# Optimization experiments

Hardware: AMD Instinct MI355X
Metric: run time of the kernel (lower is better)

Reference implementation:

```python
import jax, jax.numpy as jnp
import numpy as np

N, T, D, H, NH, BS = 4, 4096, 512, 8, 4, 64
DH = D // H                 # head dim = 64
NB = T // BS                # n_buckets = 64
CS = NH * NB                # chunk_size = 256
L = NH * T                  # sorted sequence length per head


def setup_inputs() -> dict:
    key = jax.random.key(0)
    ks = jax.random.split(key, 4)
    x = jax.random.normal(ks[0], (N, T, D), jnp.float32)
    W_Q = jax.random.normal(ks[1], (D, D), jnp.float32) * (D ** -0.5)
    W_V = jax.random.normal(ks[2], (D, D), jnp.float32) * (D ** -0.5)
    b_Q = jnp.zeros((D,), jnp.float32)
    b_V = jnp.zeros((D,), jnp.float32)
    gamma = jnp.ones((D,), jnp.float32)
    beta = jnp.zeros((D,), jnp.float32)
    # per-head random rotations: (dim_head, num_hashes, n_buckets // 2)
    rotations = jax.random.normal(ks[3], (H, DH, NH, NB // 2), jnp.float32)
    return {"x": x, "W_Q": W_Q, "b_Q": b_Q, "W_V": W_V, "b_V": b_V,
            "gamma": gamma, "beta": beta, "rotations": rotations}


def _look_one_back(a):
    # concat each chunk with the previous chunk (wrap-around for chunk 0)
    extra = jnp.concatenate([a[:, -1:], a[:, :-1]], axis=1)
    return jnp.concatenate([a, extra], axis=2)


def _lsh_head(qk, v, rot):
    # qk, v: [N, T, DH]; rot: [DH, NH, NB//2]
    rotated = jnp.einsum('btf,fhi->bhti', qk, rot)               # [N,NH,T,NB//2]
    rotated = jnp.concatenate([rotated, -rotated], axis=-1)       # [N,NH,T,NB]
    buckets = jnp.argmax(rotated, axis=-1)                        # [N,NH,T]
    offsets = (jnp.arange(NH) * NB)[None, :, None]
    buckets = (buckets + offsets).reshape(N, L)                   # [N, NH*T]

    ticker = jnp.broadcast_to(jnp.arange(L)[None, :], (N, L))
    buckets_and_t = T * buckets + (ticker % T)                    # unique keys
    sticker = jnp.argsort(buckets_and_t, axis=-1)                 # sorted ticker ids
    undo_sort = jnp.argsort(sticker, axis=-1)
    st = sticker % T                                              # original positions

    sqk = jnp.take_along_axis(qk, st[..., None], axis=1)          # [N,L,DH]
    sv = jnp.take_along_axis(v, st[..., None], axis=1)

    bq_t = st.reshape(N, CS, -1)                                  # [N,CS,BS]
    bqk = sqk.reshape(N, CS, -1, DH)
    bv = sv.reshape(N, CS, -1, DH)
    bq = bqk
    bk = bqk / (jnp.linalg.norm(bqk, axis=-1, keepdims=True) + 1e-6)

    bk = _look_one_back(bk)                                       # [N,CS,2*BS,DH]
    bv = _look_one_back(bv)
    bkv_t = _look_one_back(bq_t)

    dots = jnp.einsum('bcie,bcje->bcij', bq, bk) * (DH ** -0.5)   # [N,CS,BS,2BS]

    # mask out pairs hashed to different buckets
    q_sb = jnp.take_along_axis(buckets, sticker, axis=1).reshape(N, CS, -1)
    kv_sb = _look_one_back(q_sb)
    dots = jnp.where(q_sb[:, :, :, None] != kv_sb[:, :, None, :], -1e9, dots)
    # down-weight self-attention (same position)
    dots = jnp.where(bq_t[:, :, :, None] == bkv_t[:, :, None, :], -1e-5, dots)

    lse = jax.nn.logsumexp(dots, axis=-1, keepdims=True)
    probs = jnp.exp(dots - lse)
    bo = jnp.einsum('bcij,bcje->bcie', probs, bv)                 # [N,CS,BS,DH]

    so = bo.reshape(N, L, DH)
    slog = lse.reshape(N, L)
    o = jnp.take_along_axis(so, undo_sort[..., None], axis=1)
    logits = jnp.take_along_axis(slog, undo_sort, axis=1)

    o = o.reshape(N, NH, T, DH)
    logits = logits.reshape(N, NH, T, 1)
    pw = jnp.exp(logits - jax.nn.logsumexp(logits, axis=1, keepdims=True))
    return jnp.sum(o * pw, axis=1)                                # [N,T,DH]


def reference(x, W_Q, b_Q, W_V, b_V, gamma, beta, rotations):
    Q = x @ W_Q + b_Q
    V = x @ W_V + b_V
    Qh = Q.reshape(N, T, H, DH).transpose(2, 0, 1, 3)             # [H,N,T,DH]
    Vh = V.reshape(N, T, H, DH).transpose(2, 0, 1, 3)
    outs = jax.vmap(_lsh_head)(Qh, Vh, rotations)                 # [H,N,T,DH]
    out = outs.transpose(1, 2, 0, 3).reshape(N, T, D)
    mu = out.mean(axis=-1, keepdims=True)
    var = out.var(axis=-1, keepdims=True)
    return gamma * (out - mu) / jnp.sqrt(var + 1e-3) + beta
```

## Files before the change

### kernel.cpp

```cpp
#include <hip/hip_runtime.h>
#include <hip/hip_bf16.h>

#define N_ 4
#define T_ 4096
#define D_ 512
#define H_ 8
#define DH_ 64
#define NH_ 4
#define NB_ 64
#define CS_ 256
#define L_ 16384

typedef unsigned short u16;
typedef unsigned int u32;
typedef __attribute__((ext_vector_type(8))) short short8;
typedef __attribute__((ext_vector_type(8))) _Float16 half8;
typedef __attribute__((ext_vector_type(4))) float f32x4;
typedef __attribute__((ext_vector_type(2))) float f32x2;

__device__ __forceinline__ u16 f2bf(float x){
    union { float f; u32 u; } c; c.f = x;
    u32 u = c.u;
    u32 r = (u + 0x7FFFu + ((u >> 16) & 1u)) >> 16;
    return (u16)r;
}
__device__ __forceinline__ float bf2f(u16 b){
    union { u32 u; float f; } c; c.u = ((u32)b) << 16;
    return c.f;
}
__device__ __forceinline__ u16 f2h(float x){
    _Float16 h = (_Float16)x;
    u16 r; __builtin_memcpy(&r, &h, 2); return r;
}

#define PK_LO(acc, a, b) \
    asm("v_pk_fma_f32 %0, %1, %2, %0 op_sel:[0,0,0] op_sel_hi:[0,1,1]" \
        : "+v"(acc) : "v"(a), "v"(b))
#define PK_HI(acc, a, b) \
    asm("v_pk_fma_f32 %0, %1, %2, %0 op_sel:[1,0,0] op_sel_hi:[1,1,1]" \
        : "+v"(acc) : "v"(a), "v"(b))

#define VSWZ(d) ((((d) >> 3) ^ ((d) & 7)))

__global__ __launch_bounds__(256) void k_decXf(const float* __restrict__ x,
        u16* __restrict__ xf){
    int i = blockIdx.x * 256 + threadIdx.x;
    float4 v = ((const float4*)x)[i];
    ushort4 o;
    o.x = f2h(v.x); o.y = f2h(v.y); o.z = f2h(v.z); o.w = f2h(v.w);
    ((ushort4*)xf)[i] = o;
}

__global__ __launch_bounds__(256) void k_decWv(const float* __restrict__ Wv,
        u16* __restrict__ wvt){
    __shared__ float tile[32][33];
    const int tid = threadIdx.x;
    const int kt = blockIdx.x * 32, nt = blockIdx.y * 32;
    const int tx = tid & 31, ty = tid >> 5;
    #pragma unroll
    for (int i = 0; i < 4; ++i)
        tile[ty + i * 8][tx] = Wv[(size_t)(kt + ty + i * 8) * 512 + nt + tx];
    __syncthreads();
    #pragma unroll
    for (int i = 0; i < 4; ++i){
        int n = ty + i * 8;
        wvt[(size_t)(nt + n) * 512 + kt + tx] = f2h(tile[tx][n]);
    }
}

__global__ __launch_bounds__(512, 4) void k_q(const float* __restrict__ x,
        const float* __restrict__ Wq, const float* __restrict__ bq,
        float* __restrict__ Q, u16* __restrict__ Qbf, float* __restrict__ qinv){
    __shared__ float sA[2][16][132];
    __shared__ float sB[2][16][132];
    const int tid = threadIdx.x;
    const int tx = tid & 31, ty = tid >> 5;
    const int mb = blockIdx.x * 128, nb = blockIdx.y * 128;

    f32x2 acc2[8][2];
    #pragma unroll
    for (int i = 0; i < 8; ++i){
        acc2[i][0] = (f32x2){0.f, 0.f};
        acc2[i][1] = (f32x2){0.f, 0.f};
    }

    const int mA = tid >> 2, kA = (tid & 3) * 4;
    const int kB = tid >> 5, cB = (tid & 31) * 4;
    const float* xp = &x[(size_t)(mb + mA) * 512 + kA];
    const float* wp = &Wq[(size_t)kB * 512 + nb + cB];

    float4 pa = *(const float4*)xp;
    float4 pb = *(const float4*)wp;

    for (int k0 = 0; k0 < 512; k0 += 16){
        const int p = (k0 >> 4) & 1;
        sA[p][kA + 0][mA] = pa.x; sA[p][kA + 1][mA] = pa.y;
        sA[p][kA + 2][mA] = pa.z; sA[p][kA + 3][mA] = pa.w;
        *(float4*)&sB[p][kB][cB] = pb;
        __syncthreads();
        if (k0 < 496){
            pa = *(const float4*)(xp + k0 + 16);
            pb = *(const float4*)(wp + (size_t)(k0 + 16) * 512);
        }
        #pragma unroll
        for (int kk = 0; kk < 16; ++kk){
            float4 va0 = *(const float4*)&sA[p][kk][ty * 8];
            float4 va1 = *(const float4*)&sA[p][kk][ty * 8 + 4];
            float4 vb  = *(const float4*)&sB[p][kk][tx * 4];
            f32x2 a2[4], b2[2];
            a2[0] = (f32x2){va0.x, va0.y}; a2[1] = (f32x2){va0.z, va0.w};
            a2[2] = (f32x2){va1.x, va1.y}; a2[3] = (f32x2){va1.z, va1.w};
            b2[0] = (f32x2){vb.x, vb.y};   b2[1] = (f32x2){vb.z, vb.w};
            #pragma unroll
            for (int i = 0; i < 8; ++i){
                if (i & 1){
                    PK_HI(acc2[i][0], a2[i >> 1], b2[0]);
                    PK_HI(acc2[i][1], a2[i >> 1], b2[1]);
                } else {
                    PK_LO(acc2[i][0], a2[i >> 1], b2[0]);
                    PK_LO(acc2[i][1], a2[i >> 1], b2[1]);
                }
            }
        }
    }

    float4 vbq = *(const float4*)&bq[nb + tx * 4];
    const int h = blockIdx.y * 2 + (tx >> 4);
    const int d0 = (tx & 15) * 4;
    #pragma unroll
    for (int i = 0; i < 8; ++i){
        float o0 = acc2[i][0].x + vbq.x;
        float o1 = acc2[i][0].y + vbq.y;
        float o2 = acc2[i][1].x + vbq.z;
        float o3 = acc2[i][1].y + vbq.w;
        int m = mb + ty * 8 + i;
        int n = m >> 12, t = m & (T_ - 1);
        float4 q4; q4.x = o0; q4.y = o1; q4.z = o2; q4.w = o3;
        *(float4*)&Q[(size_t)m * 512 + nb + tx * 4] = q4;
        float ss = o0 * o0 + o1 * o1 + o2 * o2 + o3 * o3;
        #pragma unroll
        for (int s = 8; s >= 1; s >>= 1) ss += __shfl_xor(ss, s, 64);
        size_t rowb = (size_t)(h * N_ + n) * T_ + t;
        if ((tx & 15) == 0) qinv[rowb] = 1.f / (sqrtf(ss) + 1e-6f);
        ushort4 qb4;
        qb4.x = f2bf(o0); qb4.y = f2bf(o1); qb4.z = f2bf(o2); qb4.w = f2bf(o3);
        *(ushort4*)&Qbf[rowb * 64 + d0] = qb4;
    }
}

__global__ __launch_bounds__(256) void k_gemmV(const u16* __restrict__ xf,
        const u16* __restrict__ wvt, const float* __restrict__ bv,
        u16* __restrict__ Vbf){
    __shared__ __align__(16) u16 sA[128 * 40];
    __shared__ __align__(16) u16 sB[128 * 40];
    const int tid = threadIdx.x;
    const int mb = blockIdx.x * 128, nb = blockIdx.y * 128;
    const int w = tid >> 6, lane = tid & 63, quad = lane >> 4, cc = lane & 15;
    const int wm = (w & 1) * 64, wn = (w >> 1) * 64;
    f32x4 acc[4][4];
    #pragma unroll
    for (int i = 0; i < 4; ++i)
        #pragma unroll
        for (int j = 0; j < 4; ++j) acc[i][j] = (f32x4){0.f, 0.f, 0.f, 0.f};

    for (int k0 = 0; k0 < 512; k0 += 32){
        #pragma unroll
        for (int i = 0; i < 2; ++i){
            int idx = i * 256 + tid;
            int m = idx >> 2, ks = idx & 3;
            *(short8*)&sA[m * 40 + ks * 8] =
                *(const short8*)&xf[(size_t)(mb + m) * 512 + k0 + ks * 8];
            *(short8*)&sB[m * 40 + ks * 8] =
                *(const short8*)&wvt[(size_t)(nb + m) * 512 + k0 + ks * 8];
        }
        __syncthreads();
        half8 a[4], b[4];
        #pragma unroll
        for (int i = 0; i < 4; ++i){
            a[i] = *(const half8*)&sA[(wm + i * 16 + cc) * 40 + quad * 8];
            b[i] = *(const half8*)&sB[(wn + i * 16 + cc) * 40 + quad * 8];
        }
        #pragma unroll
        for (int i = 0; i < 4; ++i)
            #pragma unroll
            for (int j = 0; j < 4; ++j)
                acc[i][j] = __builtin_amdgcn_mfma_f32_16x16x32_f16(a[i], b[j], acc[i][j], 0, 0, 0);
        __syncthreads();
    }
    #pragma unroll
    for (int i = 0; i < 4; ++i)
        #pragma unroll
        for (int j = 0; j < 4; ++j){
            int c = nb + wn + j * 16 + cc;
            int hh = c >> 6, d = c & 63;
            float bi = bv[c];
            #pragma unroll
            for (int r = 0; r < 4; ++r){
                int m = mb + wm + i * 16 + quad * 4 + r;
                int n = m >> 12, t = m & (T_ - 1);
                Vbf[((size_t)(hh * N_ + n) * T_ + t) * 64 + d] = f2bf(acc[i][j][r] + bi);
            }
        }
}

__global__ __launch_bounds__(256) void k_rot(const float* __restrict__ Q,
        const float* __restrict__ rot, int* __restrict__ buckets){
    const int tb = blockIdx.x * 32;
    const int n = blockIdx.y, h = blockIdx.z;
    const int hn = h * N_ + n;
    __shared__ float Rs[64 * 128];
    __shared__ float Qs[32][64];
    const int tid = threadIdx.x;
    const float* rh = rot + (size_t)h * (64 * 128);
    for (int idx = tid; idx < 8192; idx += 256){
        int f = idx >> 7, rem = idx & 127, jj = rem >> 5, i2 = rem & 31;
        Rs[f * 128 + i2 * 4 + jj] = rh[idx];
    }
    for (int i = tid; i < 2048; i += 256){
        int t = i >> 6, f = i & 63;
        Qs[t][f] = Q[(size_t)(n * T_ + tb + t) * 512 + h * 64 + f];
    }
    __syncthreads();
    const int tx = tid & 31, tg = tid >> 5;
    f32x2 r2[4][2];
    #pragma unroll
    for (int tt = 0; tt < 4; ++tt){
        r2[tt][0] = (f32x2){0.f, 0.f};
        r2[tt][1] = (f32x2){0.f, 0.f};
    }
    for (int f = 0; f < 64; f += 2){
        f32x2 qf[4];
        #pragma unroll
        for (int tt = 0; tt < 4; ++tt)
            qf[tt] = *(const f32x2*)&Qs[tg * 4 + tt][f];
        float4 rv0 = *(const float4*)&Rs[f * 128 + tx * 4];
        float4 rv1 = *(const float4*)&Rs[(f + 1) * 128 + tx * 4];
        f32x2 b0[2], b1[2];
        b0[0] = (f32x2){rv0.x, rv0.y}; b0[1] = (f32x2){rv0.z, rv0.w};
        b1[0] = (f32x2){rv1.x, rv1.y}; b1[1] = (f32x2){rv1.z, rv1.w};
        #pragma unroll
        for (int tt = 0; tt < 4; ++tt){
            PK_LO(r2[tt][0], qf[tt], b0[0]);
            PK_LO(r2[tt][1], qf[tt], b0[1]);
            PK_HI(r2[tt][0], qf[tt], b1[0]);
            PK_HI(r2[tt][1], qf[tt], b1[1]);
        }
    }
    #pragma unroll
    for (int tt = 0; tt < 4; ++tt){
        #pragma unroll
        for (int jj = 0; jj < 4; ++jj){
            float rval = (jj < 2) ? r2[tt][0][jj] : r2[tt][1][jj - 2];
            float bv = rval; int bi = tx;
            float nv = -bv;
            if (nv > bv){ bv = nv; bi = 32 + tx; }
            #pragma unroll
            for (int m = 16; m >= 1; m >>= 1){
                float ov = __shfl_xor(bv, m, 32);
                int   oi = __shfl_xor(bi, m, 32);
                if (ov > bv || (ov == bv && oi < bi)){ bv = ov; bi = oi; }
            }
            if (tx == 0){
                int t = tb + tg * 4 + tt;
                buckets[(size_t)hn * L_ + jj * T_ + t] = bi + jj * 64;
            }
        }
    }
}

__global__ __launch_bounds__(256) void k_hist(const int* __restrict__ buckets,
        int* __restrict__ hist){
    const int tile = blockIdx.x, hn = blockIdx.y;
    const int tid = threadIdx.x;
    __shared__ int h[256];
    h[tid] = 0;
    __syncthreads();
    int b = buckets[(size_t)hn * L_ + tile * 256 + tid];
    atomicAdd(&h[b], 1);
    __syncthreads();
    hist[((size_t)hn * 64 + tile) * 256 + tid] = h[tid];
}

__global__ __launch_bounds__(256) void k_scan(int* __restrict__ hist,
        int* __restrict__ bucketStart){
    const int hn = blockIdx.x;
    const int b = threadIdx.x;
    int* hh = hist + (size_t)hn * 64 * 256;
    int run = 0;
    for (int tl = 0; tl < 64; ++tl){
        int v = hh[tl * 256 + b];
        hh[tl * 256 + b] = run;
        run += v;
    }
    __shared__ int s[256];
    s[b] = run;
    __syncthreads();
    for (int off = 1; off < 256; off <<= 1){
        int add = (b >= off) ? s[b - off] : 0;
        __syncthreads();
        s[b] += add;
        __syncthreads();
    }
    bucketStart[hn * 256 + b] = s[b] - run;
}

__global__ __launch_bounds__(256) void k_scatter(const int* __restrict__ buckets,
        const int* __restrict__ offs, const int* __restrict__ bucketStart,
        int* __restrict__ sticker){
    const int tile = blockIdx.x, hn = blockIdx.y;
    const int tid = threadIdx.x;
    __shared__ int sb[256];
    const int i = tile * 256 + tid;
    const int b = buckets[(size_t)hn * L_ + i];
    sb[tid] = b;
    __syncthreads();
    int rank = 0;
    #pragma unroll 8
    for (int j = 0; j < 256; ++j){
        int v = sb[j];
        rank += (j < tid && v == b) ? 1 : 0;
    }
    int pos = bucketStart[hn * 256 + b]
            + offs[((size_t)hn * 64 + tile) * 256 + b]
            + rank;
    sticker[(size_t)hn * L_ + pos] = i;
}

__global__ __launch_bounds__(256) void k_attn(const u16* __restrict__ Qbf,
        const u16* __restrict__ Vbf, const float* __restrict__ qinv,
        const int* __restrict__ buckets, const int* __restrict__ sticker,
        u16* __restrict__ o_hash, float* __restrict__ logit_hash){
    const int blk_c = blockIdx.x, n = blockIdx.y, h = blockIdx.z;
    const int hn = h * N_ + n;
    const int tid = threadIdx.x;
    const int w = tid >> 6, lane = tid & 63;
    const int quad = lane >> 4, cc = lane & 15;

    __shared__ __align__(16) u16 sQP[128 * 64];
    __shared__ __align__(16) u16 sVt[64 * 128];
    __shared__ int s_idx[128], s_buck[128], s_t[128];
    __shared__ float s_inv[128];
    __shared__ float s_lse[64];
    u16* const sQ = sQP;
    u16* const sP = sQP;

    if (tid < 128){
        int cprev = (blk_c + CS_ - 1) & (CS_ - 1);
        int pos = (tid < 64) ? blk_c * 64 + tid : cprev * 64 + (tid - 64);
        int idx = sticker[(size_t)hn * L_ + pos];
        s_idx[tid] = idx;
        s_buck[tid] = buckets[(size_t)hn * L_ + idx];
        int t = idx & (T_ - 1);
        s_t[tid] = t;
        s_inv[tid] = qinv[(size_t)hn * T_ + t] * 0.125f;
    }
    __syncthreads();

    const int r0 = tid >> 3, l8 = tid & 7;
    #pragma unroll
    for (int it = 0; it < 4; ++it){
        int r = it * 32 + r0;
        size_t gb = ((size_t)hn * T_ + s_t[r]) * 64 + l8 * 8;
        short8 qv = *(const short8*)&Qbf[gb];
        *(short8*)&sQ[r * 64 + ((l8 ^ (r & 7)) * 8)] = qv;
        short8 vv = *(const short8*)&Vbf[gb];
        #pragma unroll
        for (int i = 0; i < 8; ++i){
            int d = l8 * 8 + i;
            sVt[d * 128 + (((r >> 3) ^ VSWZ(d)) * 8) + (r & 7)] = (u16)vv[i];
        }
    }
    __syncthreads();

    f32x4 dacc[8];
    #pragma unroll
    for (int j = 0; j < 8; ++j) dacc[j] = (f32x4){0.f, 0.f, 0.f, 0.f};
    const int qrow = w * 16 + cc;
    #pragma unroll
    for (int kc = 0; kc < 2; ++kc){
        short8 afrag = *(const short8*)&sQ[qrow * 64 + (((kc * 4 + quad) ^ (cc & 7)) * 8)];
        #pragma unroll
        for (int kt = 0; kt < 8; ++kt){
            int krow = kt * 16 + cc;
            short8 bfrag = *(const short8*)&sQ[krow * 64 + (((kc * 4 + quad) ^ (cc & 7)) * 8)];
            dacc[kt] = __builtin_amdgcn_mfma_f32_16x16x32_bf16(afrag, bfrag, dacc[kt], 0, 0, 0);
        }
    }

    int bq[4], tq[4];
    #pragma unroll
    for (int r = 0; r < 4; ++r){
        int q = w * 16 + quad * 4 + r;
        bq[r] = s_buck[q]; tq[r] = s_t[q];
    }
    float mrow[4] = {-1e30f, -1e30f, -1e30f, -1e30f};
    #pragma unroll
    for (int kt = 0; kt < 8; ++kt){
        int kk = kt * 16 + cc;
        float inv = s_inv[kk];
        int bk = s_buck[kk], tk = s_t[kk];
        #pragma unroll
        for (int r = 0; r < 4; ++r){
            float d = dacc[kt][r] * inv;
            if (bk != bq[r]) d = -1e9f;
            if (tk == tq[r]) d = -1e-5f;
            dacc[kt][r] = d;
            mrow[r] = fmaxf(mrow[r], d);
        }
    }
    #pragma unroll
    for (int r = 0; r < 4; ++r)
        #pragma unroll
        for (int m = 8; m >= 1; m >>= 1)
            mrow[r] = fmaxf(mrow[r], __shfl_xor(mrow[r], m, 64));
    float srow[4] = {0.f, 0.f, 0.f, 0.f};
    #pragma unroll
    for (int kt = 0; kt < 8; ++kt)
        #pragma unroll
        for (int r = 0; r < 4; ++r){
            float e = __expf(dacc[kt][r] - mrow[r]);
            dacc[kt][r] = e;
            srow[r] += e;
        }
    #pragma unroll
    for (int r = 0; r < 4; ++r)
        #pragma unroll
        for (int m = 8; m >= 1; m >>= 1)
            srow[r] += __shfl_xor(srow[r], m, 64);
    float lse[4], pscale[4];
    #pragma unroll
    for (int r = 0; r < 4; ++r){
        lse[r] = mrow[r] + __logf(srow[r]);
        pscale[r] = 1.f / srow[r];
    }
    if (cc == 0){
        #pragma unroll
        for (int r = 0; r < 4; ++r) s_lse[w * 16 + quad * 4 + r] = lse[r];
    }

    __syncthreads();

    #pragma unroll
    for (int kt = 0; kt < 8; ++kt){
        int kk = kt * 16 + cc;
        #pragma unroll
        for (int r = 0; r < 4; ++r){
            int q = w * 16 + quad * 4 + r;
            sP[q * 128 + (((kk >> 3) ^ (q & 15)) * 8) + (kk & 7)] =
                f2bf(dacc[kt][r] * pscale[r]);
        }
    }
    __syncthreads();

    f32x4 oacc[4];
    #pragma unroll
    for (int j = 0; j < 4; ++j) oacc[j] = (f32x4){0.f, 0.f, 0.f, 0.f};
    #pragma unroll
    for (int kc = 0; kc < 4; ++kc){
        short8 afrag = *(const short8*)&sP[qrow * 128 + (((kc * 4 + quad) ^ cc) * 8)];
        #pragma unroll
        for (int nt = 0; nt < 4; ++nt){
            int d = nt * 16 + cc;
            short8 bfrag = *(const short8*)&sVt[d * 128 + (((kc * 4 + quad) ^ VSWZ(d)) * 8)];
            oacc[nt] = __builtin_amdgcn_mfma_f32_16x16x32_bf16(afrag, bfrag, oacc[nt], 0, 0, 0);
        }
    }

    #pragma unroll
    for (int r = 0; r < 4; ++r){
        int q = w * 16 + quad * 4 + r;
        int si = s_idx[q];
        int jj = si >> 12; int t = si & (T_ - 1);
        size_t base = ((size_t)(hn * NH_ + jj) * T_ + t) * 64;
        #pragma unroll
        for (int nt = 0; nt < 4; ++nt)
            o_hash[base + nt * 16 + cc] = f2bf(oacc[nt][r]);
    }
    if (tid < 64){
        int si = s_idx[tid]; int jj = si >> 12; int t = si & (T_ - 1);
        logit_hash[(size_t)(hn * NH_ + jj) * T_ + t] = s_lse[tid];
    }
}

__global__ __launch_bounds__(256) void k_comb(const u16* __restrict__ o_hash,
        const float* __restrict__ logit_hash, const float* __restrict__ gamma,
        const float* __restrict__ beta, float* __restrict__ out){
    const int t = blockIdx.x, n = blockIdx.y;
    const int tid = threadIdx.x;
    __shared__ float s_pw[32];
    __shared__ float s_x[512];
    __shared__ float s_red[8];
    __shared__ float s_mu, s_rs;
    if (tid < 32){
        int h = tid >> 2, j = tid & 3;
        s_pw[tid] = logit_hash[(size_t)((h * N_ + n) * NH_ + j) * T_ + t];
    }
    __syncthreads();
    if (tid < 8){
        int h = tid;
        float m = -1e30f;
        #pragma unroll
        for (int j = 0; j < 4; ++j) m = fmaxf(m, s_pw[h * 4 + j]);
        float l = 0.f;
        #pragma unroll
        for (int j = 0; j < 4; ++j) l += __expf(s_pw[h * 4 + j] - m);
        float ls = m + __logf(l);
        #pragma unroll
        for (int j = 0; j < 4; ++j) s_pw[h * 4 + j] = __expf(s_pw[h * 4 + j] - ls);
    }
    __syncthreads();
    float va[2];
    #pragma unroll
    for (int i = 0; i < 2; ++i){
        int cidx = tid + i * 256;
        int h = cidx >> 6, d = cidx & 63;
        size_t base = (size_t)((h * N_ + n) * NH_) * T_ * 64;
        float acc = 0.f;
        #pragma unroll
        for (int j = 0; j < 4; ++j)
            acc += s_pw[h * 4 + j] * bf2f(o_hash[base + ((size_t)j * T_ + t) * 64 + d]);
        s_x[cidx] = acc; va[i] = acc;
    }
    float s1 = va[0] + va[1];
    float s2 = va[0] * va[0] + va[1] * va[1];
    #pragma unroll
    for (int m = 32; m >= 1; m >>= 1){
        s1 += __shfl_xor(s1, m, 64);
        s2 += __shfl_xor(s2, m, 64);
    }
    const int lane = tid & 63, w = tid >> 6;
    if (lane == 0){ s_red[w] = s1; s_red[4 + w] = s2; }
    __syncthreads();
    if (tid == 0){
        float S1 = s_red[0] + s_red[1] + s_red[2] + s_red[3];
        float S2 = s_red[4] + s_red[5] + s_red[6] + s_red[7];
        float mu = S1 / 512.f;
        float var = S2 / 512.f - mu * mu;
        s_mu = mu; s_rs = 1.f / sqrtf(var + 1e-3f);
    }
    __syncthreads();
    #pragma unroll
    for (int i = 0; i < 2; ++i){
        int cidx = tid + i * 256;
        out[((size_t)(n * T_ + t)) * 512 + cidx] =
            gamma[cidx] * (s_x[cidx] - s_mu) * s_rs + beta[cidx];
    }
}

extern "C" void kernel_launch(void* const* d_in, const int* in_sizes, int n_in,
                              void* d_out, int out_size, void* d_ws, size_t ws_size,
                              hipStream_t stream){
    const float* x     = (const float*)d_in[0];
    const float* Wq    = (const float*)d_in[1];
    const float* bq    = (const float*)d_in[2];
    const float* Wv    = (const float*)d_in[3];
    const float* bv    = (const float*)d_in[4];
    const float* gamma = (const float*)d_in[5];
    const float* beta  = (const float*)d_in[6];
    const float* rot   = (const float*)d_in[7];
    char* ws = (char*)d_ws;
    float* Q        = (float*)(ws + 0);
    u16*   o_hash   = (u16*)  (ws + 0);
    u16*   Qbf      = (u16*)  (ws + 67108864);
    u16*   Vbf      = (u16*)  (ws + 83886080);
    float* qinv     = (float*)(ws + 100663296);
    int*   buckets  = (int*)  (ws + 101187584);
    int*   sticker  = (int*)  (ws + 103284736);
    float* logit    = (float*)(ws + 105381888);
    int*   hist     = (int*)  (ws + 107479040);
    int*   bstart   = (int*)  (ws + 109576192);
    u16*   xf       = (u16*)  (ws + 109608960);
    u16*   wvt      = (u16*)  (ws + 126386176);

    hipLaunchKernelGGL(k_decXf,   dim3(8192),       dim3(256), 0, stream,
                       x, xf);
    hipLaunchKernelGGL(k_decWv,   dim3(16, 16),     dim3(256), 0, stream,
                       Wv, wvt);
    hipLaunchKernelGGL(k_gemmV,   dim3(128, 4),     dim3(256), 0, stream,
                       xf, wvt, bv, Vbf);
    hipLaunchKernelGGL(k_q,       dim3(128, 4),     dim3(512), 0, stream,
                       x, Wq, bq, Q, Qbf, qinv);
    hipLaunchKernelGGL(k_rot,     dim3(128, 4, 8),  dim3(256), 0, stream,
                       Q, rot, buckets);
    hipLaunchKernelGGL(k_hist,    dim3(64, 32),     dim3(256), 0, stream,
                       buckets, hist);
    hipLaunchKernelGGL(k_scan,    dim3(32),         dim3(256), 0, stream,
                       hist, bstart);
    hipLaunchKernelGGL(k_scatter, dim3(64, 32),     dim3(256), 0, stream,
                       buckets, hist, bstart, sticker);
    hipLaunchKernelGGL(k_attn,    dim3(256, 4, 8),  dim3(256), 0, stream,
                       Qbf, Vbf, qinv, buckets, sticker, o_hash, logit);
    hipLaunchKernelGGL(k_comb,    dim3(4096, 4),    dim3(256), 0, stream,
                       o_hash, logit, gamma, beta, (float*)d_out);
}
```

Measured before the change: 381.0 us.

## Fuse LSH rotation and bucket argmax into the Q projection epilogue

The Q GEMM kernel now keeps its fp32 output tile in shared memory and computes the random-rotation projections and bucket argmax for its two heads directly, removing the separate rotation kernel. This drops the fp32 Q write to global memory and its re-read, plus one kernel launch. In exchange the Q kernel uses more shared memory and adds per-block reloads of the rotation matrices and extra synchronisation, which may reduce occupancy.

```diff
diff --git a/kernel.cpp b/kernel.cpp
--- a/kernel.cpp
+++ b/kernel.cpp
@@ -70,12 +70,20 @@
 
 __global__ __launch_bounds__(512, 4) void k_q(const float* __restrict__ x,
         const float* __restrict__ Wq, const float* __restrict__ bq,
-        float* __restrict__ Q, u16* __restrict__ Qbf, float* __restrict__ qinv){
-    __shared__ float sA[2][16][132];
-    __shared__ float sB[2][16][132];
+        const float* __restrict__ rot, u16* __restrict__ Qbf,
+        float* __restrict__ qinv, int* __restrict__ buckets){
+    __shared__ __align__(16) float uLDS[16640];
+    typedef float (*panel_t)[16][132];
+    panel_t sA = (panel_t)uLDS;
+    panel_t sB = (panel_t)(uLDS + 4224);
+    typedef float (*qs_t)[132];
+    qs_t Qs = (qs_t)uLDS;
+    float* Rs = uLDS + 8448;
+
     const int tid = threadIdx.x;
     const int tx = tid & 31, ty = tid >> 5;
     const int mb = blockIdx.x * 128, nb = blockIdx.y * 128;
+    const int h0 = blockIdx.y * 2;
 
     f32x2 acc2[8][2];
     #pragma unroll
@@ -125,26 +133,102 @@
     }
 
     float4 vbq = *(const float4*)&bq[nb + tx * 4];
-    const int h = blockIdx.y * 2 + (tx >> 4);
-    const int d0 = (tx & 15) * 4;
     #pragma unroll
     for (int i = 0; i < 8; ++i){
-        float o0 = acc2[i][0].x + vbq.x;
-        float o1 = acc2[i][0].y + vbq.y;
-        float o2 = acc2[i][1].x + vbq.z;
-        float o3 = acc2[i][1].y + vbq.w;
-        int m = mb + ty * 8 + i;
-        int n = m >> 12, t = m & (T_ - 1);
-        float4 q4; q4.x = o0; q4.y = o1; q4.z = o2; q4.w = o3;
-        *(float4*)&Q[(size_t)m * 512 + nb + tx * 4] = q4;
-        float ss = o0 * o0 + o1 * o1 + o2 * o2 + o3 * o3;
-        #pragma unroll
-        for (int s = 8; s >= 1; s >>= 1) ss += __shfl_xor(ss, s, 64);
-        size_t rowb = (size_t)(h * N_ + n) * T_ + t;
-        if ((tx & 15) == 0) qinv[rowb] = 1.f / (sqrtf(ss) + 1e-6f);
-        ushort4 qb4;
-        qb4.x = f2bf(o0); qb4.y = f2bf(o1); qb4.z = f2bf(o2); qb4.w = f2bf(o3);
-        *(ushort4*)&Qbf[rowb * 64 + d0] = qb4;
+        acc2[i][0].x += vbq.x; acc2[i][0].y += vbq.y;
+        acc2[i][1].x += vbq.z; acc2[i][1].y += vbq.w;
+    }
+
+    {
+        const int h = h0 + (tx >> 4);
+        const int d0 = (tx & 15) * 4;
+        #pragma unroll
+        for (int i = 0; i < 8; ++i){
+            float o0 = acc2[i][0].x, o1 = acc2[i][0].y;
+            float o2 = acc2[i][1].x, o3 = acc2[i][1].y;
+            int m = mb + ty * 8 + i;
+            int n = m >> 12, t = m & (T_ - 1);
+            float ss = o0 * o0 + o1 * o1 + o2 * o2 + o3 * o3;
+            #pragma unroll
+            for (int s = 8; s >= 1; s >>= 1) ss += __shfl_xor(ss, s, 64);
+            size_t rowb = (size_t)(h * N_ + n) * T_ + t;
+            if ((tx & 15) == 0) qinv[rowb] = 1.f / (sqrtf(ss) + 1e-6f);
+            ushort4 qb4;
+            qb4.x = f2bf(o0); qb4.y = f2bf(o1); qb4.z = f2bf(o2); qb4.w = f2bf(o3);
+            *(ushort4*)&Qbf[rowb * 64 + d0] = qb4;
+        }
+    }
+
+    __syncthreads();
+    const int gi = tid & 31, gg = tid >> 5;
+    #pragma unroll
+    for (int chunk = 0; chunk < 2; ++chunk){
+        if ((ty >> 3) == chunk){
+            const int lt0 = (ty & 7) * 8;
+            #pragma unroll
+            for (int i = 0; i < 8; ++i){
+                float4 q4;
+                q4.x = acc2[i][0].x; q4.y = acc2[i][0].y;
+                q4.z = acc2[i][1].x; q4.w = acc2[i][1].y;
+                *(float4*)&Qs[lt0 + i][tx * 4] = q4;
+            }
+        }
+        #pragma unroll
+        for (int head = 0; head < 2; ++head){
+            const float* rh = rot + (size_t)(h0 + head) * 8192;
+            for (int idx = tid; idx < 8192; idx += 512){
+                int f = idx >> 7, rem = idx & 127, jj = rem >> 5, i2 = rem & 31;
+                Rs[f * 128 + i2 * 4 + jj] = rh[idx];
+            }
+            __syncthreads();
+            f32x2 r2[4][2];
+            #pragma unroll
+            for (int tt = 0; tt < 4; ++tt){
+                r2[tt][0] = (f32x2){0.f, 0.f};
+                r2[tt][1] = (f32x2){0.f, 0.f};
+            }
+            for (int f = 0; f < 64; f += 2){
+                f32x2 qf[4];
+                #pragma unroll
+                for (int tt = 0; tt < 4; ++tt)
+                    qf[tt] = *(const f32x2*)&Qs[gg * 4 + tt][head * 64 + f];
+                float4 rv0 = *(const float4*)&Rs[f * 128 + gi * 4];
+                float4 rv1 = *(const float4*)&Rs[(f + 1) * 128 + gi * 4];
+                f32x2 b0[2], b1[2];
+                b0[0] = (f32x2){rv0.x, rv0.y}; b0[1] = (f32x2){rv0.z, rv0.w};
+                b1[0] = (f32x2){rv1.x, rv1.y}; b1[1] = (f32x2){rv1.z, rv1.w};
+                #pragma unroll
+                for (int tt = 0; tt < 4; ++tt){
+                    PK_LO(r2[tt][0], qf[tt], b0[0]);
+                    PK_LO(r2[tt][1], qf[tt], b0[1]);
+                    PK_HI(r2[tt][0], qf[tt], b1[0]);
+                    PK_HI(r2[tt][1], qf[tt], b1[1]);
+                }
+            }
+            #pragma unroll
+            for (int tt = 0; tt < 4; ++tt){
+                #pragma unroll
+                for (int jj = 0; jj < 4; ++jj){
+                    float rval = (jj < 2) ? r2[tt][0][jj] : r2[tt][1][jj - 2];
+                    float bv = rval; int bi = gi;
+                    float nv = -bv;
+                    if (nv > bv){ bv = nv; bi = 32 + gi; }
+                    #pragma unroll
+                    for (int m = 16; m >= 1; m >>= 1){
+                        float ov = __shfl_xor(bv, m, 32);
+                        int   oi = __shfl_xor(bi, m, 32);
+                        if (ov > bv || (ov == bv && oi < bi)){ bv = ov; bi = oi; }
+                    }
+                    if (gi == 0){
+                        int m = mb + chunk * 64 + gg * 4 + tt;
+                        int nn = m >> 12, t = m & (T_ - 1);
+                        buckets[(size_t)((h0 + head) * N_ + nn) * L_ + jj * T_ + t]
+                            = bi + jj * 64;
+                    }
+                }
+            }
+            __syncthreads();
+        }
     }
 }
 
@@ -201,71 +285,6 @@
                 Vbf[((size_t)(hh * N_ + n) * T_ + t) * 64 + d] = f2bf(acc[i][j][r] + bi);
             }
         }
-}
-
-__global__ __launch_bounds__(256) void k_rot(const float* __restrict__ Q,
-        const float* __restrict__ rot, int* __restrict__ buckets){
-    const int tb = blockIdx.x * 32;
-    const int n = blockIdx.y, h = blockIdx.z;
-    const int hn = h * N_ + n;
-    __shared__ float Rs[64 * 128];
-    __shared__ float Qs[32][64];
-    const int tid = threadIdx.x;
-    const float* rh = rot + (size_t)h * (64 * 128);
-    for (int idx = tid; idx < 8192; idx += 256){
-        int f = idx >> 7, rem = idx & 127, jj = rem >> 5, i2 = rem & 31;
-        Rs[f * 128 + i2 * 4 + jj] = rh[idx];
-    }
-    for (int i = tid; i < 2048; i += 256){
-        int t = i >> 6, f = i & 63;
-        Qs[t][f] = Q[(size_t)(n * T_ + tb + t) * 512 + h * 64 + f];
-    }
-    __syncthreads();
-    const int tx = tid & 31, tg = tid >> 5;
-    f32x2 r2[4][2];
-    #pragma unroll
-    for (int tt = 0; tt < 4; ++tt){
-        r2[tt][0] = (f32x2){0.f, 0.f};
-        r2[tt][1] = (f32x2){0.f, 0.f};
-    }
-    for (int f = 0; f < 64; f += 2){
-        f32x2 qf[4];
-        #pragma unroll
-        for (int tt = 0; tt < 4; ++tt)
-            qf[tt] = *(const f32x2*)&Qs[tg * 4 + tt][f];
-        float4 rv0 = *(const float4*)&Rs[f * 128 + tx * 4];
-        float4 rv1 = *(const float4*)&Rs[(f + 1) * 128 + tx * 4];
-        f32x2 b0[2], b1[2];
-        b0[0] = (f32x2){rv0.x, rv0.y}; b0[1] = (f32x2){rv0.z, rv0.w};
-        b1[0] = (f32x2){rv1.x, rv1.y}; b1[1] = (f32x2){rv1.z, rv1.w};
-        #pragma unroll
-        for (int tt = 0; tt < 4; ++tt){
-            PK_LO(r2[tt][0], qf[tt], b0[0]);
-            PK_LO(r2[tt][1], qf[tt], b0[1]);
-            PK_HI(r2[tt][0], qf[tt], b1[0]);
-            PK_HI(r2[tt][1], qf[tt], b1[1]);
-        }
-    }
-    #pragma unroll
-    for (int tt = 0; tt < 4; ++tt){
-        #pragma unroll
-        for (int jj = 0; jj < 4; ++jj){
-            float rval = (jj < 2) ? r2[tt][0][jj] : r2[tt][1][jj - 2];
-            float bv = rval; int bi = tx;
-            float nv = -bv;
-            if (nv > bv){ bv = nv; bi = 32 + tx; }
-            #pragma unroll
-            for (int m = 16; m >= 1; m >>= 1){
-                float ov = __shfl_xor(bv, m, 32);
-                int   oi = __shfl_xor(bi, m, 32);
-                if (ov > bv || (ov == bv && oi < bi)){ bv = ov; bi = oi; }
-            }
-            if (tx == 0){
-                int t = tb + tg * 4 + tt;
-                buckets[(size_t)hn * L_ + jj * T_ + t] = bi + jj * 64;
-            }
-        }
-    }
 }
 
 __global__ __launch_bounds__(256) void k_hist(const int* __restrict__ buckets,
@@ -559,7 +578,6 @@
     const float* beta  = (const float*)d_in[6];
     const float* rot   = (const float*)d_in[7];
     char* ws = (char*)d_ws;
-    float* Q        = (float*)(ws + 0);
     u16*   o_hash   = (u16*)  (ws + 0);
     u16*   Qbf      = (u16*)  (ws + 67108864);
     u16*   Vbf      = (u16*)  (ws + 83886080);
@@ -579,9 +597,7 @@
     hipLaunchKernelGGL(k_gemmV,   dim3(128, 4),     dim3(256), 0, stream,
                        xf, wvt, bv, Vbf);
     hipLaunchKernelGGL(k_q,       dim3(128, 4),     dim3(512), 0, stream,
-                       x, Wq, bq, Q, Qbf, qinv);
-    hipLaunchKernelGGL(k_rot,     dim3(128, 4, 8),  dim3(256), 0, stream,
-                       Q, rot, buckets);
+                       x, Wq, bq, rot, Qbf, qinv, buckets);
     hipLaunchKernelGGL(k_hist,    dim3(64, 32),     dim3(256), 0, stream,
                        buckets, hist);
     hipLaunchKernelGGL(k_scan,    dim3(32),         dim3(256), 0, stream,
```

Result: slower. 392.1 us (+2.9%).

## Fuse Q and V projection GEMMs into one role-split kernel, convert x inline

Applied to the files above, without the earlier changes.

Removes the separate x-to-fp16 conversion kernel by converting fp32 x to half while staging it into LDS in the V GEMM. Merges the fp32 Q GEMM and the MFMA V GEMM into one launch whose blocks take either role based on block index, so both GEMMs can run concurrently on the device. This drops two launches and an intermediate buffer round trip. In exchange, V blocks waste half their 512 threads, the V path reads fp32 x (twice the bytes), and the shared LDS allocation may limit occupancy.

```diff
diff --git a/kernel.cpp b/kernel.cpp
--- a/kernel.cpp
+++ b/kernel.cpp
@@ -42,15 +42,6 @@
 
 #define VSWZ(d) ((((d) >> 3) ^ ((d) & 7)))
 
-__global__ __launch_bounds__(256) void k_decXf(const float* __restrict__ x,
-        u16* __restrict__ xf){
-    int i = blockIdx.x * 256 + threadIdx.x;
-    float4 v = ((const float4*)x)[i];
-    ushort4 o;
-    o.x = f2h(v.x); o.y = f2h(v.y); o.z = f2h(v.z); o.w = f2h(v.w);
-    ((ushort4*)xf)[i] = o;
-}
-
 __global__ __launch_bounds__(256) void k_decWv(const float* __restrict__ Wv,
         u16* __restrict__ wvt){
     __shared__ float tile[32][33];
@@ -68,139 +59,152 @@
     }
 }
 
-__global__ __launch_bounds__(512, 4) void k_q(const float* __restrict__ x,
+__global__ __launch_bounds__(512, 4) void k_qv(const float* __restrict__ x,
         const float* __restrict__ Wq, const float* __restrict__ bq,
-        float* __restrict__ Q, u16* __restrict__ Qbf, float* __restrict__ qinv){
-    __shared__ float sA[2][16][132];
-    __shared__ float sB[2][16][132];
-    const int tid = threadIdx.x;
-    const int tx = tid & 31, ty = tid >> 5;
-    const int mb = blockIdx.x * 128, nb = blockIdx.y * 128;
-
-    f32x2 acc2[8][2];
-    #pragma unroll
-    for (int i = 0; i < 8; ++i){
-        acc2[i][0] = (f32x2){0.f, 0.f};
-        acc2[i][1] = (f32x2){0.f, 0.f};
-    }
-
-    const int mA = tid >> 2, kA = (tid & 3) * 4;
-    const int kB = tid >> 5, cB = (tid & 31) * 4;
-    const float* xp = &x[(size_t)(mb + mA) * 512 + kA];
-    const float* wp = &Wq[(size_t)kB * 512 + nb + cB];
-
-    float4 pa = *(const float4*)xp;
-    float4 pb = *(const float4*)wp;
-
-    for (int k0 = 0; k0 < 512; k0 += 16){
-        const int p = (k0 >> 4) & 1;
-        sA[p][kA + 0][mA] = pa.x; sA[p][kA + 1][mA] = pa.y;
-        sA[p][kA + 2][mA] = pa.z; sA[p][kA + 3][mA] = pa.w;
-        *(float4*)&sB[p][kB][cB] = pb;
-        __syncthreads();
-        if (k0 < 496){
-            pa = *(const float4*)(xp + k0 + 16);
-            pb = *(const float4*)(wp + (size_t)(k0 + 16) * 512);
-        }
-        #pragma unroll
-        for (int kk = 0; kk < 16; ++kk){
-            float4 va0 = *(const float4*)&sA[p][kk][ty * 8];
-            float4 va1 = *(const float4*)&sA[p][kk][ty * 8 + 4];
-            float4 vb  = *(const float4*)&sB[p][kk][tx * 4];
-            f32x2 a2[4], b2[2];
-            a2[0] = (f32x2){va0.x, va0.y}; a2[1] = (f32x2){va0.z, va0.w};
-            a2[2] = (f32x2){va1.x, va1.y}; a2[3] = (f32x2){va1.z, va1.w};
-            b2[0] = (f32x2){vb.x, vb.y};   b2[1] = (f32x2){vb.z, vb.w};
-            #pragma unroll
-            for (int i = 0; i < 8; ++i){
-                if (i & 1){
-                    PK_HI(acc2[i][0], a2[i >> 1], b2[0]);
-                    PK_HI(acc2[i][1], a2[i >> 1], b2[1]);
-                } else {
-                    PK_LO(acc2[i][0], a2[i >> 1], b2[0]);
-                    PK_LO(acc2[i][1], a2[i >> 1], b2[1]);
+        const u16* __restrict__ wvt, const float* __restrict__ bv,
+        float* __restrict__ Q, u16* __restrict__ Qbf, float* __restrict__ qinv,
+        u16* __restrict__ Vbf){
+    __shared__ __align__(16) char uLDS[33792];
+
+    const int bid = blockIdx.x;
+    const int role = (bid >> 8) & 1;
+    const int id = ((bid >> 9) << 8) | (bid & 255);
+    const int mb = (id & 127) * 128;
+    const int nbi = id >> 7;
+    const int nb = nbi * 128;
+    const int tid = threadIdx.x;
+
+    if (role == 0){
+        typedef float (*pan_t)[16][132];
+        pan_t sA = (pan_t)uLDS;
+        pan_t sB = (pan_t)(uLDS + 16896);
+        const int tx = tid & 31, ty = tid >> 5;
+        f32x2 acc2[8][2];
+        #pragma unroll
+        for (int i = 0; i < 8; ++i){
+            acc2[i][0] = (f32x2){0.f, 0.f};
+            acc2[i][1] = (f32x2){0.f, 0.f};
+        }
+        const int mA = tid >> 2, kA = (tid & 3) * 4;
+        const int kB = tid >> 5, cB = (tid & 31) * 4;
+        const float* xp = &x[(size_t)(mb + mA) * 512 + kA];
+        const float* wp = &Wq[(size_t)kB * 512 + nb + cB];
+        float4 pa = *(const float4*)xp;
+        float4 pb = *(const float4*)wp;
+
+        for (int k0 = 0; k0 < 512; k0 += 16){
+            const int p = (k0 >> 4) & 1;
+            sA[p][kA + 0][mA] = pa.x; sA[p][kA + 1][mA] = pa.y;
+            sA[p][kA + 2][mA] = pa.z; sA[p][kA + 3][mA] = pa.w;
+            *(float4*)&sB[p][kB][cB] = pb;
+            __syncthreads();
+            if (k0 < 496){
+                pa = *(const float4*)(xp + k0 + 16);
+                pb = *(const float4*)(wp + (size_t)(k0 + 16) * 512);
+            }
+            #pragma unroll
+            for (int kk = 0; kk < 16; ++kk){
+                float4 va0 = *(const float4*)&sA[p][kk][ty * 8];
+                float4 va1 = *(const float4*)&sA[p][kk][ty * 8 + 4];
+                float4 vb  = *(const float4*)&sB[p][kk][tx * 4];
+                f32x2 a2[4], b2[2];
+                a2[0] = (f32x2){va0.x, va0.y}; a2[1] = (f32x2){va0.z, va0.w};
+                a2[2] = (f32x2){va1.x, va1.y}; a2[3] = (f32x2){va1.z, va1.w};
+                b2[0] = (f32x2){vb.x, vb.y};   b2[1] = (f32x2){vb.z, vb.w};
+                #pragma unroll
+                for (int i = 0; i < 8; ++i){
+                    if (i & 1){
+                        PK_HI(acc2[i][0], a2[i >> 1], b2[0]);
+                        PK_HI(acc2[i][1], a2[i >> 1], b2[1]);
+                    } else {
+                        PK_LO(acc2[i][0], a2[i >> 1], b2[0]);
+                        PK_LO(acc2[i][1], a2[i >> 1], b2[1]);
+                    }
                 }
             }
         }
-    }
-
-    float4 vbq = *(const float4*)&bq[nb + tx * 4];
-    const int h = blockIdx.y * 2 + (tx >> 4);
-    const int d0 = (tx & 15) * 4;
-    #pragma unroll
-    for (int i = 0; i < 8; ++i){
-        float o0 = acc2[i][0].x + vbq.x;
-        float o1 = acc2[i][0].y + vbq.y;
-        float o2 = acc2[i][1].x + vbq.z;
-        float o3 = acc2[i][1].y + vbq.w;
-        int m = mb + ty * 8 + i;
-        int n = m >> 12, t = m & (T_ - 1);
-        float4 q4; q4.x = o0; q4.y = o1; q4.z = o2; q4.w = o3;
-        *(float4*)&Q[(size_t)m * 512 + nb + tx * 4] = q4;
-        float ss = o0 * o0 + o1 * o1 + o2 * o2 + o3 * o3;
-        #pragma unroll
-        for (int s = 8; s >= 1; s >>= 1) ss += __shfl_xor(ss, s, 64);
-        size_t rowb = (size_t)(h * N_ + n) * T_ + t;
-        if ((tx & 15) == 0) qinv[rowb] = 1.f / (sqrtf(ss) + 1e-6f);
-        ushort4 qb4;
-        qb4.x = f2bf(o0); qb4.y = f2bf(o1); qb4.z = f2bf(o2); qb4.w = f2bf(o3);
-        *(ushort4*)&Qbf[rowb * 64 + d0] = qb4;
-    }
-}
-
-__global__ __launch_bounds__(256) void k_gemmV(const u16* __restrict__ xf,
-        const u16* __restrict__ wvt, const float* __restrict__ bv,
-        u16* __restrict__ Vbf){
-    __shared__ __align__(16) u16 sA[128 * 40];
-    __shared__ __align__(16) u16 sB[128 * 40];
-    const int tid = threadIdx.x;
-    const int mb = blockIdx.x * 128, nb = blockIdx.y * 128;
-    const int w = tid >> 6, lane = tid & 63, quad = lane >> 4, cc = lane & 15;
-    const int wm = (w & 1) * 64, wn = (w >> 1) * 64;
-    f32x4 acc[4][4];
-    #pragma unroll
-    for (int i = 0; i < 4; ++i)
-        #pragma unroll
-        for (int j = 0; j < 4; ++j) acc[i][j] = (f32x4){0.f, 0.f, 0.f, 0.f};
-
-    for (int k0 = 0; k0 < 512; k0 += 32){
-        #pragma unroll
-        for (int i = 0; i < 2; ++i){
-            int idx = i * 256 + tid;
-            int m = idx >> 2, ks = idx & 3;
-            *(short8*)&sA[m * 40 + ks * 8] =
-                *(const short8*)&xf[(size_t)(mb + m) * 512 + k0 + ks * 8];
-            *(short8*)&sB[m * 40 + ks * 8] =
-                *(const short8*)&wvt[(size_t)(nb + m) * 512 + k0 + ks * 8];
-        }
-        __syncthreads();
-        half8 a[4], b[4];
-        #pragma unroll
-        for (int i = 0; i < 4; ++i){
-            a[i] = *(const half8*)&sA[(wm + i * 16 + cc) * 40 + quad * 8];
-            b[i] = *(const half8*)&sB[(wn + i * 16 + cc) * 40 + quad * 8];
-        }
+
+        float4 vbq = *(const float4*)&bq[nb + tx * 4];
+        const int h = nbi * 2 + (tx >> 4);
+        const int d0 = (tx & 15) * 4;
+        #pragma unroll
+        for (int i = 0; i < 8; ++i){
+            float o0 = acc2[i][0].x + vbq.x;
+            float o1 = acc2[i][0].y + vbq.y;
+            float o2 = acc2[i][1].x + vbq.z;
+            float o3 = acc2[i][1].y + vbq.w;
+            int m = mb + ty * 8 + i;
+            int n = m >> 12, t = m & (T_ - 1);
+            float4 q4; q4.x = o0; q4.y = o1; q4.z = o2; q4.w = o3;
+            *(float4*)&Q[(size_t)m * 512 + nb + tx * 4] = q4;
+            float ss = o0 * o0 + o1 * o1 + o2 * o2 + o3 * o3;
+            #pragma unroll
+            for (int s = 8; s >= 1; s >>= 1) ss += __shfl_xor(ss, s, 64);
+            size_t rowb = (size_t)(h * N_ + n) * T_ + t;
+            if ((tx & 15) == 0) qinv[rowb] = 1.f / (sqrtf(ss) + 1e-6f);
+            ushort4 qb4;
+            qb4.x = f2bf(o0); qb4.y = f2bf(o1); qb4.z = f2bf(o2); qb4.w = f2bf(o3);
+            *(ushort4*)&Qbf[rowb * 64 + d0] = qb4;
+        }
+    } else {
+        if (tid >= 256) return;
+        u16* sA = (u16*)uLDS;
+        u16* sB = (u16*)(uLDS + 10240);
+        const int w = tid >> 6, lane = tid & 63;
+        const int quad = lane >> 4, cc = lane & 15;
+        const int wm = (w & 1) * 64, wn = (w >> 1) * 64;
+        f32x4 acc[4][4];
         #pragma unroll
         for (int i = 0; i < 4; ++i)
             #pragma unroll
-            for (int j = 0; j < 4; ++j)
-                acc[i][j] = __builtin_amdgcn_mfma_f32_16x16x32_f16(a[i], b[j], acc[i][j], 0, 0, 0);
-        __syncthreads();
-    }
-    #pragma unroll
-    for (int i = 0; i < 4; ++i)
-        #pragma unroll
-        for (int j = 0; j < 4; ++j){
-            int c = nb + wn + j * 16 + cc;
-            int hh = c >> 6, d = c & 63;
-            float bi = bv[c];
-            #pragma unroll
-            for (int r = 0; r < 4; ++r){
-                int m = mb + wm + i * 16 + quad * 4 + r;
-                int n = m >> 12, t = m & (T_ - 1);
-                Vbf[((size_t)(hh * N_ + n) * T_ + t) * 64 + d] = f2bf(acc[i][j][r] + bi);
-            }
-        }
+            for (int j = 0; j < 4; ++j) acc[i][j] = (f32x4){0.f, 0.f, 0.f, 0.f};
+
+        for (int k0 = 0; k0 < 512; k0 += 32){
+            #pragma unroll
+            for (int i = 0; i < 2; ++i){
+                int idx = i * 256 + tid;
+                int m = idx >> 2, ks = idx & 3;
+                const float* xs = &x[(size_t)(mb + m) * 512 + k0 + ks * 8];
+                float4 f0 = *(const float4*)xs;
+                float4 f1 = *(const float4*)(xs + 4);
+                short8 s;
+                s[0] = (short)f2h(f0.x); s[1] = (short)f2h(f0.y);
+                s[2] = (short)f2h(f0.z); s[3] = (short)f2h(f0.w);
+                s[4] = (short)f2h(f1.x); s[5] = (short)f2h(f1.y);
+                s[6] = (short)f2h(f1.z); s[7] = (short)f2h(f1.w);
+                *(short8*)&sA[m * 40 + ks * 8] = s;
+                *(short8*)&sB[m * 40 + ks * 8] =
+                    *(const short8*)&wvt[(size_t)(nb + m) * 512 + k0 + ks * 8];
+            }
+            __syncthreads();
+            half8 a[4], b[4];
+            #pragma unroll
+            for (int i = 0; i < 4; ++i){
+                a[i] = *(const half8*)&sA[(wm + i * 16 + cc) * 40 + quad * 8];
+                b[i] = *(const half8*)&sB[(wn + i * 16 + cc) * 40 + quad * 8];
+            }
+            #pragma unroll
+            for (int i = 0; i < 4; ++i)
+                #pragma unroll
+                for (int j = 0; j < 4; ++j)
+                    acc[i][j] = __builtin_amdgcn_mfma_f32_16x16x32_f16(a[i], b[j], acc[i][j], 0, 0, 0);
+            __syncthreads();
+        }
+        #pragma unroll
+        for (int i = 0; i < 4; ++i)
+            #pragma unroll
+            for (int j = 0; j < 4; ++j){
+                int c = nb + wn + j * 16 + cc;
+                int hh = c >> 6, d = c & 63;
+                float bi = bv[c];
+                #pragma unroll
+                for (int r = 0; r < 4; ++r){
+                    int m = mb + wm + i * 16 + quad * 4 + r;
+                    int n = m >> 12, t = m & (T_ - 1);
+                    Vbf[((size_t)(hh * N_ + n) * T_ + t) * 64 + d] = f2bf(acc[i][j][r] + bi);
+                }
+            }
+    }
 }
 
 __global__ __launch_bounds__(256) void k_rot(const float* __restrict__ Q,
@@ -569,17 +573,12 @@
     float* logit    = (float*)(ws + 105381888);
     int*   hist     = (int*)  (ws + 107479040);
     int*   bstart   = (int*)  (ws + 109576192);
-    u16*   xf       = (u16*)  (ws + 109608960);
-    u16*   wvt      = (u16*)  (ws + 126386176);
-
-    hipLaunchKernelGGL(k_decXf,   dim3(8192),       dim3(256), 0, stream,
-                       x, xf);
+    u16*   wvt      = (u16*)  (ws + 109608960);
+
     hipLaunchKernelGGL(k_decWv,   dim3(16, 16),     dim3(256), 0, stream,
                        Wv, wvt);
-    hipLaunchKernelGGL(k_gemmV,   dim3(128, 4),     dim3(256), 0, stream,
-                       xf, wvt, bv, Vbf);
-    hipLaunchKernelGGL(k_q,       dim3(128, 4),     dim3(512), 0, stream,
-                       x, Wq, bq, Q, Qbf, qinv);
+    hipLaunchKernelGGL(k_qv,      dim3(1024),       dim3(512), 0, stream,
+                       x, Wq, bq, wvt, bv, Q, Qbf, qinv, Vbf);
     hipLaunchKernelGGL(k_rot,     dim3(128, 4, 8),  dim3(256), 0, stream,
                        Q, rot, buckets);
     hipLaunchKernelGGL(k_hist,    dim3(64, 32),     dim3(256), 0, stream,
```

Measured after the change: 380.7 us. No clear change (-0.1%).
